# Kernel optimization log

Measured on AMD Instinct MI355X. Metric: run time of the kernel, lower is better.

Reference implementation:

```python
import jax, jax.numpy as jnp
import numpy as np

B, N, D_IN, E, H = 4, 512, 256, 64, 4
NEG = 1.0e9


def setup_inputs() -> dict:
    key = jax.random.key(0)
    ks = jax.random.split(key, 7)
    s = 1.0 / np.sqrt(D_IN)  # dense-init scale
    return {
        "x": jax.random.normal(ks[0], (B, N, D_IN), jnp.float32),
        "Wq": jax.random.normal(ks[1], (H, D_IN, E), jnp.float32) * s,
        "bq": jnp.zeros((H, E), jnp.float32),
        "Wk": jax.random.normal(ks[2], (H, D_IN, E), jnp.float32) * s,
        "bk": jnp.zeros((H, E), jnp.float32),
        "Wv": jax.random.normal(ks[3], (H, D_IN, E), jnp.float32) * s,
        "bv": jnp.zeros((H, E), jnp.float32),
    }


def _sdp(q, k, v):
    logits = jnp.einsum('bne,bme->bnm', q, k) / jnp.sqrt(jnp.asarray(E, q.dtype))
    return jnp.einsum('bnm,bme->bne', jax.nn.softmax(logits, axis=-1), v)


def _cosine(q, k, v):
    qn = q / jnp.linalg.norm(q, axis=-1, keepdims=True)
    kn = k / jnp.linalg.norm(k, axis=-1, keepdims=True)
    logits = jnp.einsum('bne,bme->bnm', qn, kn)
    return jnp.einsum('bnm,bme->bne', jax.nn.softmax(logits, axis=-1), v)


def _l1(q, k, v):
    # [B,N,N] L1 distances via broadcasted [B,N,N,E] diff, as in the original
    d = jnp.sum(jnp.abs(q[:, :, None, :] - k[:, None, :, :]), axis=-1)
    return jnp.einsum('bnm,bme->bne', jax.nn.softmax(-d, axis=-1), v)


def _l2(q, k, v):
    d = jnp.sqrt(jnp.sum(jnp.square(q[:, :, None, :] - k[:, None, :, :]), axis=-1))
    return jnp.einsum('bnm,bme->bne', jax.nn.softmax(-d, axis=-1), v)


_HEAD_FNS = (_sdp, _cosine, _l1, _l2)  # attention_types per head


def reference(x, Wq, bq, Wk, bk, Wv, bv):
    # Per-head projections: [B,H,N,E]
    q = jnp.einsum('bnd,hde->bhne', x, Wq) + bq[None, :, None, :]
    k = jnp.einsum('bnd,hde->bhne', x, Wk) + bk[None, :, None, :]
    v = jnp.einsum('bnd,hde->bhne', x, Wv) + bv[None, :, None, :]
    outs = [fn(q[:, h], k[:, h], v[:, h]) for h, fn in enumerate(_HEAD_FNS)]
    return jnp.concatenate(outs, axis=-1)  # [B,N,H*E]
```

## Files before the change

### kernel.cpp

```cpp
#include <hip/hip_runtime.h>
#include <hip/hip_bf16.h>
#include <math.h>

#define B_   4
#define N_   512
#define DIN  256
#define E_   64
#define H_   4

typedef __attribute__((ext_vector_type(8))) short bf16x8;
typedef __attribute__((ext_vector_type(8))) unsigned short u16x8;
typedef __attribute__((ext_vector_type(4))) float f32x4;

__device__ __forceinline__ unsigned short f2bf(float f) {
    __hip_bfloat16 h = __float2bfloat16(f);
    return *reinterpret_cast<unsigned short*>(&h);
}
__device__ __forceinline__ int slot2bh(int slot) {
    return ((slot & 7) << 1) | (slot >> 3);
}

__global__ __launch_bounds__(256) void proj_kernel(
    const float* __restrict__ x,
    const float* __restrict__ Wq, const float* __restrict__ bq,
    const float* __restrict__ Wk, const float* __restrict__ bk,
    const float* __restrict__ Wv, const float* __restrict__ bv,
    float* __restrict__ Q, float* __restrict__ KT,
    float* __restrict__ qn2, float* __restrict__ kn2,
    unsigned short* __restrict__ QF, unsigned short* __restrict__ KF,
    unsigned short* __restrict__ VF)
{
    const int tid = threadIdx.x;
    const int slot = blockIdx.x & 15;
    const int rest = blockIdx.x >> 4;
    const int tile = rest & 15;
    const int p    = rest >> 4;
    const int bhid = slot2bh(slot);
    const int h = bhid & 3;
    const int b = bhid >> 2;

    const float* W;
    const float* bias;
    if (p == 0)      { W = Wq; bias = bq; }
    else if (p == 1) { W = Wk; bias = bk; }
    else             { W = Wv; bias = bv; }
    W    += (size_t)h * DIN * E_;
    bias += h * E_;

    const int rowbase = tile * 32;
    const float* xb = x + ((size_t)b * N_ + rowbase) * DIN;

    __shared__ float XsT[64][34];
    __shared__ float Ws[64][64];
    __shared__ float Ys[64][33];
    __shared__ unsigned short Vst[64][48];

    const int tr = tid >> 4;
    const int tc = tid & 15;

    float acc[2][4];
    #pragma unroll
    for (int i = 0; i < 2; ++i)
        #pragma unroll
        for (int j = 0; j < 4; ++j) acc[i][j] = 0.f;

    for (int dc = 0; dc < DIN; dc += 64) {
        for (int l = tid; l < 2048; l += 256) {
            int r = l >> 6, d = l & 63;
            XsT[d][r] = xb[r * DIN + dc + d];
        }
        {
            const float4* Wg4 = (const float4*)(W + (size_t)dc * E_);
            #pragma unroll
            for (int i = 0; i < 4; ++i) ((float4*)Ws)[tid + i * 256] = Wg4[tid + i * 256];
        }
        __syncthreads();

        #pragma unroll 8
        for (int d = 0; d < 64; ++d) {
            float2 xv = *(const float2*)&XsT[d][tr * 2];
            float4 wv = *(const float4*)&Ws[d][tc * 4];
            acc[0][0] = fmaf(xv.x, wv.x, acc[0][0]);
            acc[0][1] = fmaf(xv.x, wv.y, acc[0][1]);
            acc[0][2] = fmaf(xv.x, wv.z, acc[0][2]);
            acc[0][3] = fmaf(xv.x, wv.w, acc[0][3]);
            acc[1][0] = fmaf(xv.y, wv.x, acc[1][0]);
            acc[1][1] = fmaf(xv.y, wv.y, acc[1][1]);
            acc[1][2] = fmaf(xv.y, wv.z, acc[1][2]);
            acc[1][3] = fmaf(xv.y, wv.w, acc[1][3]);
        }
        __syncthreads();
    }

    const size_t bh = (size_t)bhid;
    float4 bias4 = *(const float4*)&bias[tc * 4];
    float v0[4], v1[4];
    v0[0] = acc[0][0] + bias4.x; v0[1] = acc[0][1] + bias4.y;
    v0[2] = acc[0][2] + bias4.z; v0[3] = acc[0][3] + bias4.w;
    v1[0] = acc[1][0] + bias4.x; v1[1] = acc[1][1] + bias4.y;
    v1[2] = acc[1][2] + bias4.z; v1[3] = acc[1][3] + bias4.w;

    const int r0 = rowbase + tr * 2;

    if (p < 2) {
        float s0 = 0.f, s1 = 0.f;
        #pragma unroll
        for (int j = 0; j < 4; ++j) {
            s0 = fmaf(v0[j], v0[j], s0);
            s1 = fmaf(v1[j], v1[j], s1);
        }
        #pragma unroll
        for (int off = 1; off < 16; off <<= 1) {
            s0 += __shfl_xor(s0, off, 64);
            s1 += __shfl_xor(s1, off, 64);
        }
        if (tc == 0) {
            float* nrm = (p == 0) ? qn2 : kn2;
            nrm[bh * N_ + r0]     = s0;
            nrm[bh * N_ + r0 + 1] = s1;
        }
        unsigned short* f = ((p == 0) ? QF : KF) + bh * (size_t)(N_ * E_);
        const int t_ = r0 >> 4, li = r0 & 15;
        const int gg = tc >> 1, j0 = (tc & 1) * 4;
        ushort4 u0, u1;
        u0.x = f2bf(v0[0]); u0.y = f2bf(v0[1]); u0.z = f2bf(v0[2]); u0.w = f2bf(v0[3]);
        u1.x = f2bf(v1[0]); u1.y = f2bf(v1[1]); u1.z = f2bf(v1[2]); u1.w = f2bf(v1[3]);
        *(ushort4*)&f[(size_t)((t_ * 8 + gg) * 16 + li) * 8 + j0]       = u0;
        *(ushort4*)&f[(size_t)((t_ * 8 + gg) * 16 + li + 1) * 8 + j0]   = u1;
    }

    if (p == 0) {
        if (h == 2) {
            float* o = Q + bh * (size_t)(N_ * E_);
            *(float4*)&o[(size_t)r0 * E_ + tc * 4]       = make_float4(v0[0], v0[1], v0[2], v0[3]);
            *(float4*)&o[(size_t)(r0 + 1) * E_ + tc * 4] = make_float4(v1[0], v1[1], v1[2], v1[3]);
        }
    } else if (p == 1) {
        if (h == 2) {
            #pragma unroll
            for (int j = 0; j < 4; ++j) {
                Ys[tc * 4 + j][tr * 2]     = v0[j];
                Ys[tc * 4 + j][tr * 2 + 1] = v1[j];
            }
            __syncthreads();
            const int e  = tid >> 2;
            const int n0 = (tid & 3) * 8;
            float* o = KT + bh * (size_t)(E_ * N_) + (size_t)e * N_ + rowbase + n0;
            float4 a, c;
            a.x = Ys[e][n0 + 0]; a.y = Ys[e][n0 + 1];
            a.z = Ys[e][n0 + 2]; a.w = Ys[e][n0 + 3];
            c.x = Ys[e][n0 + 4]; c.y = Ys[e][n0 + 5];
            c.z = Ys[e][n0 + 6]; c.w = Ys[e][n0 + 7];
            *(float4*)&o[0] = a;
            *(float4*)&o[4] = c;
        }
    } else {
        #pragma unroll
        for (int j = 0; j < 4; ++j) {
            Vst[tc * 4 + j][tr * 2]     = f2bf(v0[j]);
            Vst[tc * 4 + j][tr * 2 + 1] = f2bf(v1[j]);
        }
        __syncthreads();
        const int et = tid >> 6, g = (tid >> 4) & 3, li = tid & 15;
        u16x8 wv8 = *(const u16x8*)&Vst[et * 16 + li][g * 8];
        *(u16x8*)&VF[bh * (size_t)(N_ * E_)
                     + (size_t)((((tile * 4 + et) * 4 + g) * 16) + li) * 8] = wv8;
    }
}

template <int HEAD>
__device__ __forceinline__ void mfma_logits32(
    int w, int kh, int lane, size_t bh, int qt, int q0, int pid,
    const unsigned short* __restrict__ QF,
    const unsigned short* __restrict__ KF,
    const float* __restrict__ qn2, const float* __restrict__ kn2,
    char* Pw, float* __restrict__ Mpart, float* __restrict__ Spart)
{
    const int g = lane >> 4, li = lane & 15;
    const int row0 = g * 4;
    const unsigned short* qfb = QF + bh * (N_ * E_) + (size_t)qt * 1024;
    const unsigned short* kfb = KF + bh * (N_ * E_);

    bf16x8 a0 = *(const bf16x8*)&qfb[(g * 16 + li) * 8];
    bf16x8 a1 = *(const bf16x8*)&qfb[((g + 4) * 16 + li) * 8];

    float qrow[4];
    if (HEAD == 1) {
        #pragma unroll
        for (int j = 0; j < 4; ++j) qrow[j] = rsqrtf(qn2[bh * N_ + q0 + row0 + j]);
    } else if (HEAD == 3) {
        #pragma unroll
        for (int j = 0; j < 4; ++j) qrow[j] = qn2[bh * N_ + q0 + row0 + j];
    }

    float lg[2][4];
    #pragma unroll
    for (int t = 0; t < 2; ++t) {
        const int kt = (kh * 4 + w) * 2 + t;
        const int m0 = kt * 16;
        bf16x8 b0 = *(const bf16x8*)&kfb[(size_t)((kt * 8 + g) * 16 + li) * 8];
        bf16x8 b1 = *(const bf16x8*)&kfb[(size_t)((kt * 8 + g + 4) * 16 + li) * 8];
        f32x4 acc = {0.f, 0.f, 0.f, 0.f};
        acc = __builtin_amdgcn_mfma_f32_16x16x32_bf16(a0, b0, acc, 0, 0, 0);
        acc = __builtin_amdgcn_mfma_f32_16x16x32_bf16(a1, b1, acc, 0, 0, 0);
        float kcol = 0.f, rk = 0.f;
        if (HEAD == 1) { kcol = kn2[bh * N_ + m0 + li]; rk = rsqrtf(kcol); }
        if (HEAD == 3) { kcol = kn2[bh * N_ + m0 + li]; }
        #pragma unroll
        for (int j = 0; j < 4; ++j) {
            float d = acc[j];
            if (HEAD == 0)      lg[t][j] = d * 0.125f;
            else if (HEAD == 1) lg[t][j] = d * qrow[j] * rk;
            else                lg[t][j] = -sqrtf(fmaxf(qrow[j] + kcol - 2.f * d, 0.f));
        }
    }

    float mx[4];
    #pragma unroll
    for (int j = 0; j < 4; ++j) {
        float m = fmaxf(lg[0][j], lg[1][j]);
        #pragma unroll
        for (int off = 1; off < 16; off <<= 1) m = fmaxf(m, __shfl_xor(m, off, 64));
        mx[j] = m;
    }

    float sm[4] = {0.f, 0.f, 0.f, 0.f};
    #pragma unroll
    for (int t = 0; t < 2; ++t) {
        #pragma unroll
        for (int j = 0; j < 4; ++j) {
            const int row = row0 + j;
            float pv = __expf(lg[t][j] - mx[j]);
            sm[j] += pv;
            const int byte = (row * 64 + (t * 16 + li) * 2) ^ ((row & 7) << 4);
            *(unsigned short*)(Pw + byte) = f2bf(pv);
        }
    }
    #pragma unroll
    for (int j = 0; j < 4; ++j) {
        float s = sm[j];
        #pragma unroll
        for (int off = 1; off < 16; off <<= 1) s += __shfl_xor(s, off, 64);
        if (li == 0) {
            Mpart[(size_t)pid * 16 + row0 + j] = mx[j];
            Spart[(size_t)pid * 16 + row0 + j] = s;
        }
    }
}

__global__ __launch_bounds__(256) void attn_partial(
    const float* __restrict__ Qf, const float* __restrict__ KT,
    const unsigned short* __restrict__ QF, const unsigned short* __restrict__ KF,
    const unsigned short* __restrict__ VF,
    const float* __restrict__ qn2, const float* __restrict__ kn2,
    float* __restrict__ Opart, float* __restrict__ Mpart,
    float* __restrict__ Spart)
{
    const int tid  = threadIdx.x;
    const int w    = tid >> 6;
    const int lane = tid & 63;
    const int slot  = blockIdx.x & 15;
    const int inner = blockIdx.x >> 4;
    const int kh = inner & 3;
    const int qt = inner >> 2;
    const int bhid = slot2bh(slot);
    const size_t bhs = (size_t)bhid;
    const int q0 = qt * 16;
    const int pid = bhid * 512 + qt * 16 + kh * 4 + w;

    __shared__ unsigned short Plds[4][512];
    __shared__ float q_lds[16][68];

    const int g = lane >> 4, li = lane & 15;
    char* Pw = (char*)&Plds[w][0];
    const int h = bhid & 3;

    if (h == 2) {
        {
            const int r = tid >> 4, c0 = (tid & 15) * 4;
            *(float4*)&q_lds[r][c0] =
                *(const float4*)&Qf[bhs * (N_ * E_) + (size_t)(q0 + r) * E_ + c0];
        }
        __syncthreads();

        const int half = lane >> 5;
        const int kloc = lane & 31;
        const int key  = kh * 128 + w * 32 + kloc;
        const float* kp = KT + bhs * (E_ * N_) + key;

        float acc[8];
        #pragma unroll
        for (int i = 0; i < 8; ++i) acc[i] = 0.f;

        #pragma unroll 4
        for (int ec = 0; ec < 16; ++ec) {
            float k0 = kp[(size_t)(ec * 4 + 0) * N_];
            float k1 = kp[(size_t)(ec * 4 + 1) * N_];
            float k2 = kp[(size_t)(ec * 4 + 2) * N_];
            float k3 = kp[(size_t)(ec * 4 + 3) * N_];
            #pragma unroll
            for (int i = 0; i < 8; ++i) {
                float4 q4 = *(const float4*)&q_lds[half * 8 + i][ec * 4];
                acc[i] += fabsf(k0 - q4.x) + fabsf(k1 - q4.y)
                        + fabsf(k2 - q4.z) + fabsf(k3 - q4.w);
            }
        }

        #pragma unroll
        for (int i = 0; i < 8; ++i) {
            const int row = half * 8 + i;
            float mn = acc[i];
            #pragma unroll
            for (int off = 1; off < 32; off <<= 1) mn = fminf(mn, __shfl_xor(mn, off, 64));
            float p = __expf(mn - acc[i]);
            float s = p;
            #pragma unroll
            for (int off = 1; off < 32; off <<= 1) s += __shfl_xor(s, off, 64);
            const int byte = (row * 64 + kloc * 2) ^ ((row & 7) << 4);
            *(unsigned short*)(Pw + byte) = f2bf(p);
            if (kloc == 0) {
                Mpart[(size_t)pid * 16 + row] = -mn;
                Spart[(size_t)pid * 16 + row] = s;
            }
        }
    } else if (h == 0) {
        mfma_logits32<0>(w, kh, lane, bhs, qt, q0, pid, QF, KF, qn2, kn2, Pw, Mpart, Spart);
    } else if (h == 1) {
        mfma_logits32<1>(w, kh, lane, bhs, qt, q0, pid, QF, KF, qn2, kn2, Pw, Mpart, Spart);
    } else {
        mfma_logits32<3>(w, kh, lane, bhs, qt, q0, pid, QF, KF, qn2, kn2, Pw, Mpart, Spart);
    }
    __syncthreads();

    {
        const int byte = (li * 64 + g * 16) ^ ((li & 7) << 4);
        bf16x8 pa = *(const bf16x8*)(Pw + byte);
        const int kb = kh * 4 + w;
        const unsigned short* vfb = VF + bhs * (N_ * E_);
        #pragma unroll
        for (int et = 0; et < 4; ++et) {
            f32x4 acc = {0.f, 0.f, 0.f, 0.f};
            bf16x8 vb = *(const bf16x8*)&vfb[
                (size_t)((((kb * 4 + et) * 4 + g) * 16) + li) * 8];
            acc = __builtin_amdgcn_mfma_f32_16x16x32_bf16(pa, vb, acc, 0, 0, 0);
            *(f32x4*)&Opart[(size_t)pid * 1024 + ((et * 4 + g) * 16 + li) * 4] = acc;
        }
    }
}

__global__ __launch_bounds__(256) void combine_kernel(
    const float* __restrict__ Opart, const float* __restrict__ Mpart,
    const float* __restrict__ Spart, float* __restrict__ out)
{
    const int tid = threadIdx.x;
    const int slot = blockIdx.x & 15;
    const int qt   = blockIdx.x >> 4;
    const int bhid = slot2bh(slot);
    const int b = bhid >> 2, h = bhid & 3;
    const int base = (bhid * 32 + qt) * 16;

    __shared__ float ms[16][16], ss[16][16], wls[16][16];
    __shared__ float sginv[16];
    __shared__ float Ot[16][68];

    {
        const int p = tid >> 4, row = tid & 15;
        ms[p][row] = Mpart[(size_t)(base + p) * 16 + row];
        ss[p][row] = Spart[(size_t)(base + p) * 16 + row];
    }
    __syncthreads();
    {
        const int p = tid >> 4, row = tid & 15;
        float mg = ms[0][row];
        #pragma unroll
        for (int q = 1; q < 16; ++q) mg = fmaxf(mg, ms[q][row]);
        wls[p][row] = __expf(ms[p][row] - mg);
    }
    __syncthreads();
    if (tid < 16) {
        float s = 0.f;
        #pragma unroll
        for (int p = 0; p < 16; ++p) s += wls[p][tid] * ss[p][tid];
        sginv[tid] = 1.f / s;
    }
    __syncthreads();

    {
        const int et = tid >> 6, g = (tid >> 4) & 3, li = tid & 15;
        float o0 = 0.f, o1 = 0.f, o2 = 0.f, o3 = 0.f;
        const float* op = Opart + (size_t)base * 1024 + ((et * 4 + g) * 16 + li) * 4;
        #pragma unroll
        for (int p = 0; p < 16; ++p) {
            float4 v = *(const float4*)(op + (size_t)p * 1024);
            o0 = fmaf(wls[p][g * 4 + 0], v.x, o0);
            o1 = fmaf(wls[p][g * 4 + 1], v.y, o1);
            o2 = fmaf(wls[p][g * 4 + 2], v.z, o2);
            o3 = fmaf(wls[p][g * 4 + 3], v.w, o3);
        }
        Ot[g * 4 + 0][et * 16 + li] = o0 * sginv[g * 4 + 0];
        Ot[g * 4 + 1][et * 16 + li] = o1 * sginv[g * 4 + 1];
        Ot[g * 4 + 2][et * 16 + li] = o2 * sginv[g * 4 + 2];
        Ot[g * 4 + 3][et * 16 + li] = o3 * sginv[g * 4 + 3];
    }
    __syncthreads();
    {
        const int row = tid >> 4, e0 = (tid & 15) * 4;
        const int n = qt * 16 + row;
        *(float4*)&out[((size_t)b * N_ + n) * (H_ * E_) + h * E_ + e0] =
            *(const float4*)&Ot[row][e0];
    }
}

extern "C" void kernel_launch(void* const* d_in, const int* in_sizes, int n_in,
                              void* d_out, int out_size, void* d_ws, size_t ws_size,
                              hipStream_t stream)
{
    const float* x  = (const float*)d_in[0];
    const float* Wq = (const float*)d_in[1];
    const float* bq = (const float*)d_in[2];
    const float* Wk = (const float*)d_in[3];
    const float* bk = (const float*)d_in[4];
    const float* Wv = (const float*)d_in[5];
    const float* bv = (const float*)d_in[6];
    float* out = (float*)d_out;

    const size_t qkv = (size_t)B_ * H_ * N_ * E_;
    float* Q     = (float*)d_ws;
    float* KT    = Q + qkv;
    float* qn2   = KT + qkv;
    float* kn2   = qn2 + (size_t)B_ * H_ * N_;
    float* Opart = kn2 + (size_t)B_ * H_ * N_;
    float* Mpart = Opart + (size_t)8192 * 1024;
    float* Spart = Mpart + (size_t)8192 * 16;
    unsigned short* QF = (unsigned short*)(Spart + (size_t)8192 * 16);
    unsigned short* KF = QF + qkv;
    unsigned short* VF = KF + qkv;

    proj_kernel<<<B_ * H_ * 3 * (N_ / 32), 256, 0, stream>>>(
        x, Wq, bq, Wk, bk, Wv, bv, Q, KT, qn2, kn2, QF, KF, VF);
    attn_partial<<<B_ * H_ * 32 * 4, 256, 0, stream>>>(
        Q, KT, QF, KF, VF, qn2, kn2, Opart, Mpart, Spart);
    combine_kernel<<<B_ * H_ * 32, 256, 0, stream>>>(Opart, Mpart, Spart, out);
}
```

Before: 58.96 us.

## Fuse attention partial and combine kernels into one 1024-thread block per query tile

Merges attn_partial and combine_kernel into a single kernel with 16 waves per block, each wave handling a 32-key chunk. Per-wave max, sum and partial outputs now stay in shared memory instead of going through global Opart/Mpart/Spart buffers, and one kernel launch is removed. Partial outputs are stored in LDS as bf16, which adds some rounding error. The grid drops to 512 blocks of 1024 threads, so the larger LDS footprint may lower occupancy.

```diff
diff --git a/kernel.cpp b/kernel.cpp
--- a/kernel.cpp
+++ b/kernel.cpp
@@ -15,6 +15,10 @@
 __device__ __forceinline__ unsigned short f2bf(float f) {
     __hip_bfloat16 h = __float2bfloat16(f);
     return *reinterpret_cast<unsigned short*>(&h);
+}
+__device__ __forceinline__ float bf2f(unsigned short u) {
+    unsigned int v = ((unsigned int)u) << 16;
+    return __uint_as_float(v);
 }
 __device__ __forceinline__ int slot2bh(int slot) {
     return ((slot & 7) << 1) | (slot >> 3);
@@ -168,115 +172,36 @@
     }
 }
 
-template <int HEAD>
-__device__ __forceinline__ void mfma_logits32(
-    int w, int kh, int lane, size_t bh, int qt, int q0, int pid,
-    const unsigned short* __restrict__ QF,
-    const unsigned short* __restrict__ KF,
-    const float* __restrict__ qn2, const float* __restrict__ kn2,
-    char* Pw, float* __restrict__ Mpart, float* __restrict__ Spart)
-{
-    const int g = lane >> 4, li = lane & 15;
-    const int row0 = g * 4;
-    const unsigned short* qfb = QF + bh * (N_ * E_) + (size_t)qt * 1024;
-    const unsigned short* kfb = KF + bh * (N_ * E_);
-
-    bf16x8 a0 = *(const bf16x8*)&qfb[(g * 16 + li) * 8];
-    bf16x8 a1 = *(const bf16x8*)&qfb[((g + 4) * 16 + li) * 8];
-
-    float qrow[4];
-    if (HEAD == 1) {
-        #pragma unroll
-        for (int j = 0; j < 4; ++j) qrow[j] = rsqrtf(qn2[bh * N_ + q0 + row0 + j]);
-    } else if (HEAD == 3) {
-        #pragma unroll
-        for (int j = 0; j < 4; ++j) qrow[j] = qn2[bh * N_ + q0 + row0 + j];
-    }
-
-    float lg[2][4];
-    #pragma unroll
-    for (int t = 0; t < 2; ++t) {
-        const int kt = (kh * 4 + w) * 2 + t;
-        const int m0 = kt * 16;
-        bf16x8 b0 = *(const bf16x8*)&kfb[(size_t)((kt * 8 + g) * 16 + li) * 8];
-        bf16x8 b1 = *(const bf16x8*)&kfb[(size_t)((kt * 8 + g + 4) * 16 + li) * 8];
-        f32x4 acc = {0.f, 0.f, 0.f, 0.f};
-        acc = __builtin_amdgcn_mfma_f32_16x16x32_bf16(a0, b0, acc, 0, 0, 0);
-        acc = __builtin_amdgcn_mfma_f32_16x16x32_bf16(a1, b1, acc, 0, 0, 0);
-        float kcol = 0.f, rk = 0.f;
-        if (HEAD == 1) { kcol = kn2[bh * N_ + m0 + li]; rk = rsqrtf(kcol); }
-        if (HEAD == 3) { kcol = kn2[bh * N_ + m0 + li]; }
-        #pragma unroll
-        for (int j = 0; j < 4; ++j) {
-            float d = acc[j];
-            if (HEAD == 0)      lg[t][j] = d * 0.125f;
-            else if (HEAD == 1) lg[t][j] = d * qrow[j] * rk;
-            else                lg[t][j] = -sqrtf(fmaxf(qrow[j] + kcol - 2.f * d, 0.f));
-        }
-    }
-
-    float mx[4];
-    #pragma unroll
-    for (int j = 0; j < 4; ++j) {
-        float m = fmaxf(lg[0][j], lg[1][j]);
-        #pragma unroll
-        for (int off = 1; off < 16; off <<= 1) m = fmaxf(m, __shfl_xor(m, off, 64));
-        mx[j] = m;
-    }
-
-    float sm[4] = {0.f, 0.f, 0.f, 0.f};
-    #pragma unroll
-    for (int t = 0; t < 2; ++t) {
-        #pragma unroll
-        for (int j = 0; j < 4; ++j) {
-            const int row = row0 + j;
-            float pv = __expf(lg[t][j] - mx[j]);
-            sm[j] += pv;
-            const int byte = (row * 64 + (t * 16 + li) * 2) ^ ((row & 7) << 4);
-            *(unsigned short*)(Pw + byte) = f2bf(pv);
-        }
-    }
-    #pragma unroll
-    for (int j = 0; j < 4; ++j) {
-        float s = sm[j];
-        #pragma unroll
-        for (int off = 1; off < 16; off <<= 1) s += __shfl_xor(s, off, 64);
-        if (li == 0) {
-            Mpart[(size_t)pid * 16 + row0 + j] = mx[j];
-            Spart[(size_t)pid * 16 + row0 + j] = s;
-        }
-    }
-}
-
-__global__ __launch_bounds__(256) void attn_partial(
+__global__ __launch_bounds__(1024) void attn_fused(
     const float* __restrict__ Qf, const float* __restrict__ KT,
     const unsigned short* __restrict__ QF, const unsigned short* __restrict__ KF,
     const unsigned short* __restrict__ VF,
     const float* __restrict__ qn2, const float* __restrict__ kn2,
-    float* __restrict__ Opart, float* __restrict__ Mpart,
-    float* __restrict__ Spart)
+    float* __restrict__ out)
 {
     const int tid  = threadIdx.x;
     const int w    = tid >> 6;
     const int lane = tid & 63;
-    const int slot  = blockIdx.x & 15;
-    const int inner = blockIdx.x >> 4;
-    const int kh = inner & 3;
-    const int qt = inner >> 2;
+    const int slot = blockIdx.x & 15;
+    const int qt   = blockIdx.x >> 4;
     const int bhid = slot2bh(slot);
     const size_t bhs = (size_t)bhid;
     const int q0 = qt * 16;
-    const int pid = bhid * 512 + qt * 16 + kh * 4 + w;
-
-    __shared__ unsigned short Plds[4][512];
+    const int h = bhid & 3;
+
+    __shared__ unsigned short Plds[16][512];
     __shared__ float q_lds[16][68];
+    __shared__ unsigned short OL[16][16][66];
+    __shared__ float wmaxL[16][16];
+    __shared__ float wsumL[16][16];
+    __shared__ float wls[16][16];
+    __shared__ float sginv[16];
 
     const int g = lane >> 4, li = lane & 15;
     char* Pw = (char*)&Plds[w][0];
-    const int h = bhid & 3;
 
     if (h == 2) {
-        {
+        if (tid < 256) {
             const int r = tid >> 4, c0 = (tid & 15) * 4;
             *(float4*)&q_lds[r][c0] =
                 *(const float4*)&Qf[bhs * (N_ * E_) + (size_t)(q0 + r) * E_ + c0];
@@ -285,7 +210,7 @@
 
         const int half = lane >> 5;
         const int kloc = lane & 31;
-        const int key  = kh * 128 + w * 32 + kloc;
+        const int key  = w * 32 + kloc;
         const float* kp = KT + bhs * (E_ * N_) + key;
 
         float acc[8];
@@ -319,95 +244,123 @@
             const int byte = (row * 64 + kloc * 2) ^ ((row & 7) << 4);
             *(unsigned short*)(Pw + byte) = f2bf(p);
             if (kloc == 0) {
-                Mpart[(size_t)pid * 16 + row] = -mn;
-                Spart[(size_t)pid * 16 + row] = s;
-            }
-        }
-    } else if (h == 0) {
-        mfma_logits32<0>(w, kh, lane, bhs, qt, q0, pid, QF, KF, qn2, kn2, Pw, Mpart, Spart);
-    } else if (h == 1) {
-        mfma_logits32<1>(w, kh, lane, bhs, qt, q0, pid, QF, KF, qn2, kn2, Pw, Mpart, Spart);
+                wmaxL[w][row] = -mn;
+                wsumL[w][row] = s;
+            }
+        }
     } else {
-        mfma_logits32<3>(w, kh, lane, bhs, qt, q0, pid, QF, KF, qn2, kn2, Pw, Mpart, Spart);
-    }
-    __syncthreads();
+        const int row0 = g * 4;
+        const unsigned short* qfb = QF + bhs * (N_ * E_) + (size_t)qt * 1024;
+        const unsigned short* kfb = KF + bhs * (N_ * E_);
+
+        bf16x8 a0 = *(const bf16x8*)&qfb[(g * 16 + li) * 8];
+        bf16x8 a1 = *(const bf16x8*)&qfb[((g + 4) * 16 + li) * 8];
+
+        float qrow[4] = {0.f, 0.f, 0.f, 0.f};
+        if (h == 1) {
+            #pragma unroll
+            for (int j = 0; j < 4; ++j) qrow[j] = rsqrtf(qn2[bhs * N_ + q0 + row0 + j]);
+        } else if (h == 3) {
+            #pragma unroll
+            for (int j = 0; j < 4; ++j) qrow[j] = qn2[bhs * N_ + q0 + row0 + j];
+        }
+
+        float lg[2][4];
+        #pragma unroll
+        for (int t = 0; t < 2; ++t) {
+            const int kt = w * 2 + t;
+            const int m0 = kt * 16;
+            bf16x8 b0 = *(const bf16x8*)&kfb[(size_t)((kt * 8 + g) * 16 + li) * 8];
+            bf16x8 b1 = *(const bf16x8*)&kfb[(size_t)((kt * 8 + g + 4) * 16 + li) * 8];
+            f32x4 acc = {0.f, 0.f, 0.f, 0.f};
+            acc = __builtin_amdgcn_mfma_f32_16x16x32_bf16(a0, b0, acc, 0, 0, 0);
+            acc = __builtin_amdgcn_mfma_f32_16x16x32_bf16(a1, b1, acc, 0, 0, 0);
+            float kcol = 0.f, rk = 0.f;
+            if (h == 1) { kcol = kn2[bhs * N_ + m0 + li]; rk = rsqrtf(kcol); }
+            if (h == 3) { kcol = kn2[bhs * N_ + m0 + li]; }
+            #pragma unroll
+            for (int j = 0; j < 4; ++j) {
+                float d = acc[j];
+                if (h == 0)      lg[t][j] = d * 0.125f;
+                else if (h == 1) lg[t][j] = d * qrow[j] * rk;
+                else             lg[t][j] = -sqrtf(fmaxf(qrow[j] + kcol - 2.f * d, 0.f));
+            }
+        }
+
+        float mx[4];
+        #pragma unroll
+        for (int j = 0; j < 4; ++j) {
+            float m = fmaxf(lg[0][j], lg[1][j]);
+            #pragma unroll
+            for (int off = 1; off < 16; off <<= 1) m = fmaxf(m, __shfl_xor(m, off, 64));
+            mx[j] = m;
+        }
+
+        float sm[4] = {0.f, 0.f, 0.f, 0.f};
+        #pragma unroll
+        for (int t = 0; t < 2; ++t) {
+            #pragma unroll
+            for (int j = 0; j < 4; ++j) {
+                const int row = row0 + j;
+                float pv = __expf(lg[t][j] - mx[j]);
+                sm[j] += pv;
+                const int byte = (row * 64 + (t * 16 + li) * 2) ^ ((row & 7) << 4);
+                *(unsigned short*)(Pw + byte) = f2bf(pv);
+            }
+        }
+        #pragma unroll
+        for (int j = 0; j < 4; ++j) {
+            float s = sm[j];
+            #pragma unroll
+            for (int off = 1; off < 16; off <<= 1) s += __shfl_xor(s, off, 64);
+            if (li == 0) {
+                wmaxL[w][row0 + j] = mx[j];
+                wsumL[w][row0 + j] = s;
+            }
+        }
+    }
 
     {
         const int byte = (li * 64 + g * 16) ^ ((li & 7) << 4);
         bf16x8 pa = *(const bf16x8*)(Pw + byte);
-        const int kb = kh * 4 + w;
         const unsigned short* vfb = VF + bhs * (N_ * E_);
         #pragma unroll
         for (int et = 0; et < 4; ++et) {
             f32x4 acc = {0.f, 0.f, 0.f, 0.f};
             bf16x8 vb = *(const bf16x8*)&vfb[
-                (size_t)((((kb * 4 + et) * 4 + g) * 16) + li) * 8];
+                (size_t)((((w * 4 + et) * 4 + g) * 16) + li) * 8];
             acc = __builtin_amdgcn_mfma_f32_16x16x32_bf16(pa, vb, acc, 0, 0, 0);
-            *(f32x4*)&Opart[(size_t)pid * 1024 + ((et * 4 + g) * 16 + li) * 4] = acc;
-        }
-    }
-}
-
-__global__ __launch_bounds__(256) void combine_kernel(
-    const float* __restrict__ Opart, const float* __restrict__ Mpart,
-    const float* __restrict__ Spart, float* __restrict__ out)
-{
-    const int tid = threadIdx.x;
-    const int slot = blockIdx.x & 15;
-    const int qt   = blockIdx.x >> 4;
-    const int bhid = slot2bh(slot);
-    const int b = bhid >> 2, h = bhid & 3;
-    const int base = (bhid * 32 + qt) * 16;
-
-    __shared__ float ms[16][16], ss[16][16], wls[16][16];
-    __shared__ float sginv[16];
-    __shared__ float Ot[16][68];
-
-    {
+            #pragma unroll
+            for (int j = 0; j < 4; ++j)
+                OL[w][g * 4 + j][et * 16 + li] = f2bf(acc[j]);
+        }
+    }
+    __syncthreads();
+
+    if (tid < 256) {
         const int p = tid >> 4, row = tid & 15;
-        ms[p][row] = Mpart[(size_t)(base + p) * 16 + row];
-        ss[p][row] = Spart[(size_t)(base + p) * 16 + row];
-    }
-    __syncthreads();
-    {
-        const int p = tid >> 4, row = tid & 15;
-        float mg = ms[0][row];
-        #pragma unroll
-        for (int q = 1; q < 16; ++q) mg = fmaxf(mg, ms[q][row]);
-        wls[p][row] = __expf(ms[p][row] - mg);
+        float mg = wmaxL[0][row];
+        #pragma unroll
+        for (int q = 1; q < 16; ++q) mg = fmaxf(mg, wmaxL[q][row]);
+        wls[p][row] = __expf(wmaxL[p][row] - mg);
     }
     __syncthreads();
     if (tid < 16) {
         float s = 0.f;
         #pragma unroll
-        for (int p = 0; p < 16; ++p) s += wls[p][tid] * ss[p][tid];
+        for (int p = 0; p < 16; ++p) s += wls[p][tid] * wsumL[p][tid];
         sginv[tid] = 1.f / s;
-    }
-    __syncthreads();
-
-    {
-        const int et = tid >> 6, g = (tid >> 4) & 3, li = tid & 15;
-        float o0 = 0.f, o1 = 0.f, o2 = 0.f, o3 = 0.f;
-        const float* op = Opart + (size_t)base * 1024 + ((et * 4 + g) * 16 + li) * 4;
-        #pragma unroll
-        for (int p = 0; p < 16; ++p) {
-            float4 v = *(const float4*)(op + (size_t)p * 1024);
-            o0 = fmaf(wls[p][g * 4 + 0], v.x, o0);
-            o1 = fmaf(wls[p][g * 4 + 1], v.y, o1);
-            o2 = fmaf(wls[p][g * 4 + 2], v.z, o2);
-            o3 = fmaf(wls[p][g * 4 + 3], v.w, o3);
-        }
-        Ot[g * 4 + 0][et * 16 + li] = o0 * sginv[g * 4 + 0];
-        Ot[g * 4 + 1][et * 16 + li] = o1 * sginv[g * 4 + 1];
-        Ot[g * 4 + 2][et * 16 + li] = o2 * sginv[g * 4 + 2];
-        Ot[g * 4 + 3][et * 16 + li] = o3 * sginv[g * 4 + 3];
     }
     __syncthreads();
     {
-        const int row = tid >> 4, e0 = (tid & 15) * 4;
-        const int n = qt * 16 + row;
-        *(float4*)&out[((size_t)b * N_ + n) * (H_ * E_) + h * E_ + e0] =
-            *(const float4*)&Ot[row][e0];
+        const int row = tid >> 6, e = tid & 63;
+        float o = 0.f;
+        #pragma unroll
+        for (int p = 0; p < 16; ++p)
+            o = fmaf(wls[p][row], bf2f(OL[p][row][e]), o);
+        const int b = bhid >> 2;
+        const int n = q0 + row;
+        out[((size_t)b * N_ + n) * (H_ * E_) + h * E_ + e] = o * sginv[row];
     }
 }
 
@@ -425,20 +378,16 @@
     float* out = (float*)d_out;
 
     const size_t qkv = (size_t)B_ * H_ * N_ * E_;
-    float* Q     = (float*)d_ws;
-    float* KT    = Q + qkv;
-    float* qn2   = KT + qkv;
-    float* kn2   = qn2 + (size_t)B_ * H_ * N_;
-    float* Opart = kn2 + (size_t)B_ * H_ * N_;
-    float* Mpart = Opart + (size_t)8192 * 1024;
-    float* Spart = Mpart + (size_t)8192 * 16;
-    unsigned short* QF = (unsigned short*)(Spart + (size_t)8192 * 16);
+    float* Q   = (float*)d_ws;
+    float* KT  = Q + qkv;
+    float* qn2 = KT + qkv;
+    float* kn2 = qn2 + (size_t)B_ * H_ * N_;
+    unsigned short* QF = (unsigned short*)(kn2 + (size_t)B_ * H_ * N_);
     unsigned short* KF = QF + qkv;
     unsigned short* VF = KF + qkv;
 
     proj_kernel<<<B_ * H_ * 3 * (N_ / 32), 256, 0, stream>>>(
         x, Wq, bq, Wk, bk, Wv, bv, Q, KT, qn2, kn2, QF, KF, VF);
-    attn_partial<<<B_ * H_ * 32 * 4, 256, 0, stream>>>(
-        Q, KT, QF, KF, VF, qn2, kn2, Opart, Mpart, Spart);
-    combine_kernel<<<B_ * H_ * 32, 256, 0, stream>>>(Opart, Mpart, Spart, out);
-}
+    attn_fused<<<B_ * H_ * 32, 1024, 0, stream>>>(
+        Q, KT, QF, KF, VF, qn2, kn2, out);
+}
```

New measurement: 50.61 us, median of 3. -14.2%, faster.
